# Optimization experiments

Hardware: AMD Instinct MI355X
Metric: run time of the kernel (lower is better)

## Reference

```python
import jax, jax.numpy as jnp
import numpy as np

B, L, D = 2, 2048, 512
DI, N, K, R = 1024, 16, 4, 32  # d_inner=2*d_model, d_state, d_conv, dt_rank=ceil(512/16)
CK = 31   # conformer depthwise kernel
DFF = 2048  # feedforward_factor * d_hidden

def _ln(h, g, b):
    m = h.mean(-1, keepdims=True)
    v = ((h - m) ** 2).mean(-1, keepdims=True)
    return (h - m) * jax.lax.rsqrt(v + 1e-5) * g + b

def _dwconv(h, w, b, pad):
    # h: [B,L,C], w: [C,1,K] depthwise kernel
    y = jax.lax.conv_general_dilated(h.transpose(0, 2, 1), w, (1,), [pad],
                                     feature_group_count=h.shape[-1],
                                     dimension_numbers=('NCH', 'OIH', 'NCH'))
    return y.transpose(0, 2, 1) + b

def setup_inputs():
    key = jax.random.key(0)
    ks = jax.random.split(key, 16)
    nrm = lambda k, s, sc=0.02: jax.random.normal(k, s, jnp.float32) * sc
    return {
        'x': jax.random.normal(ks[0], (B, L, D), jnp.float32),
        'ln_g': jnp.ones(D), 'ln_b': jnp.zeros(D),
        'W_in': nrm(ks[1], (D, 2 * DI)),
        'conv_w': nrm(ks[2], (DI, 1, K), 0.1), 'conv_b': jnp.zeros(DI),
        'W_x': nrm(ks[3], (DI, R + 2 * N)),
        'W_dt': nrm(ks[4], (R, DI), 0.1), 'b_dt': nrm(ks[5], (DI,), 0.1),
        'A_log': jnp.log(jnp.broadcast_to(jnp.arange(1, N + 1, dtype=jnp.float32), (DI, N))),
        'Dp': jnp.ones(DI),
        'W_out': nrm(ks[6], (DI, D)),
        'cm_ln_g': jnp.ones(D), 'cm_ln_b': jnp.zeros(D),
        'cm_pw1_w': nrm(ks[7], (D, 2 * D)), 'cm_pw1_b': jnp.zeros(2 * D),
        'cm_dw_w': nrm(ks[8], (D, 1, CK), 0.1), 'cm_dw_b': jnp.zeros(D),
        'cm_pw2_w': nrm(ks[9], (D, D)), 'cm_pw2_b': jnp.zeros(D),
        'ff_W1': nrm(ks[10], (D, DFF)), 'ff_b1': jnp.zeros(DFF),
        'ff_W2': nrm(ks[11], (DFF, D)), 'ff_b2': jnp.zeros(D),
    }

def _forward(x, ln_g, ln_b, W_in, conv_w, conv_b, W_x, W_dt, b_dt, A_log, Dp, W_out,
             cm_ln_g, cm_ln_b, cm_pw1_w, cm_pw1_b, cm_dw_w, cm_dw_b, cm_pw2_w, cm_pw2_b,
             ff_W1, ff_b1, ff_W2, ff_b2):
    # --- pre LayerNorm ---
    h = _ln(x, ln_g, ln_b)
    # --- Mamba block ---
    xz = h @ W_in                       # [B,L,2*DI]
    xi, z = xz[..., :DI], xz[..., DI:]
    xc = jax.nn.silu(_dwconv(xi, conv_w, conv_b, (K - 1, 0)))  # causal depthwise conv
    dbl = xc @ W_x                      # [B,L,R+2N]
    dt, Bm, Cm = dbl[..., :R], dbl[..., R:R + N], dbl[..., R + N:]
    delta = jax.nn.softplus(dt @ W_dt + b_dt)           # [B,L,DI]
    A = -jnp.exp(A_log)                                  # [DI,N]
    dA = jnp.exp(delta[..., None] * A)                   # [B,L,DI,N]
    dBu = (delta * xc)[..., None] * Bm[:, :, None, :]    # [B,L,DI,N]
    def step(hs, inp):
        a, bu, c = inp
        hs = a * hs + bu                                 # [B,DI,N]
        return hs, jnp.einsum('bdn,bn->bd', hs, c)
    h0 = jnp.zeros((x.shape[0], DI, N), x.dtype)
    _, ys = jax.lax.scan(step, h0, (dA.transpose(1, 0, 2, 3), dBu.transpose(1, 0, 2, 3), Cm.transpose(1, 0, 2)))
    y = ys.transpose(1, 0, 2) + Dp * xc
    y = y * jax.nn.silu(z)
    m = y @ W_out                                        # [B,L,D]
    # --- Conformer-style conv module (residual) ---
    c = _ln(m, cm_ln_g, cm_ln_b)
    c = c @ cm_pw1_w + cm_pw1_b
    a_, g_ = jnp.split(c, 2, axis=-1)
    c = a_ * jax.nn.sigmoid(g_)  # GLU
    c = jax.nn.silu(_dwconv(c, cm_dw_w, cm_dw_b, ((CK - 1) // 2, (CK - 1) // 2)))
    c = c @ cm_pw2_w + cm_pw2_b
    m = m + c
    # --- post LayerNorm (shared params) + FFN (residual) ---
    f = _ln(m, ln_g, ln_b)
    out = f + (jax.nn.gelu(f @ ff_W1 + ff_b1) @ ff_W2 + ff_b2)
    return out

def reference(x, ln_g, ln_b, W_in, conv_w, conv_b, W_x, W_dt, b_dt, A_log, Dp, W_out,
              cm_ln_g, cm_ln_b, cm_pw1_w, cm_pw1_b, cm_dw_w, cm_dw_b, cm_pw2_w, cm_pw2_b,
              ff_W1, ff_b1, ff_W2, ff_b2):
    return _forward(x, ln_g, ln_b, W_in, conv_w, conv_b, W_x, W_dt, b_dt, A_log, Dp, W_out,
                    cm_ln_g, cm_ln_b, cm_pw1_w, cm_pw1_b, cm_dw_w, cm_dw_b, cm_pw2_w, cm_pw2_b,
                    ff_W1, ff_b1, ff_W2, ff_b2)
```

## Files before the change

### kernel.cpp

```cpp
#include <hip/hip_runtime.h>
#include <hip/hip_bf16.h>
#include <math.h>

#define Bc   2
#define Lc   2048
#define Dc   512
#define DIc  1024
#define Nc   16
#define Kc   4
#define Rc   32
#define CKc  31
#define DFFc 2048
#define Mrows (Bc*Lc)
#define CHUNK  32
#define NCHUNK 64

typedef __hip_bfloat16 bf16;
typedef short bf16x8 __attribute__((ext_vector_type(8)));
typedef float f32x4  __attribute__((ext_vector_type(4)));

__device__ __forceinline__ float sigmoidf_(float x){ return 1.f/(1.f+expf(-x)); }
__device__ __forceinline__ float siluf_(float x){ return x*sigmoidf_(x); }
__device__ __forceinline__ float softplusf_(float x){ return fmaxf(x,0.f)+log1pf(expf(-fabsf(x))); }
__device__ __forceinline__ float geluf_(float x){
    float x3 = x*x*x;
    return 0.5f*x*(1.f+tanhf(0.7978845608028654f*(x+0.044715f*x3)));
}

__device__ __forceinline__ void gload16(const void* g, void* l) {
    __builtin_amdgcn_global_load_lds((const __attribute__((address_space(1))) void*)g,
                                     (__attribute__((address_space(3))) void*)l, 16, 0, 0);
}

template<bool WF, bool WB>
__global__ void ln_kernel(const float* __restrict__ in, const float* __restrict__ g,
                          const float* __restrict__ bb, float* __restrict__ outf,
                          bf16* __restrict__ outb, int D) {
    int row = blockIdx.x;
    const float* x = in + (size_t)row * D;
    float s = 0.f, s2 = 0.f;
    for (int i = threadIdx.x; i < D; i += blockDim.x) { float v = x[i]; s += v; s2 += v*v; }
    #pragma unroll
    for (int off = 32; off; off >>= 1) { s += __shfl_down(s, off); s2 += __shfl_down(s2, off); }
    __shared__ float sh[2][4];
    int wave = threadIdx.x >> 6, lane = threadIdx.x & 63;
    if (lane == 0) { sh[0][wave] = s; sh[1][wave] = s2; }
    __syncthreads();
    if (threadIdx.x == 0) {
        float ts = 0.f, ts2 = 0.f;
        int nw = blockDim.x >> 6;
        for (int w = 0; w < nw; ++w) { ts += sh[0][w]; ts2 += sh[1][w]; }
        sh[0][0] = ts; sh[1][0] = ts2;
    }
    __syncthreads();
    float mean = sh[0][0] / D;
    float var  = sh[1][0] / D - mean*mean;
    float rstd = rsqrtf(var + 1e-5f);
    for (int i = threadIdx.x; i < D; i += blockDim.x) {
        float v = (x[i]-mean)*rstd*g[i] + bb[i];
        if (WF) outf[(size_t)row*D + i] = v;
        if (WB) outb[(size_t)row*D + i] = __float2bfloat16(v);
    }
}

struct PrepPack {
    const float* W[8]; bf16* Wt[8]; int K[8]; int N[8]; int start[9];
    const float* x; const float* lg; const float* lb; bf16* hb;
    int lnStart;
};

__global__ __launch_bounds__(256) void prep_all(PrepPack p) {
    __shared__ float t[32][33];
    __shared__ float sh[2][4];
    int tb = blockIdx.x, tid = threadIdx.x;
    if (tb < p.lnStart) {
        int wi = 0;
        #pragma unroll
        for (int i = 0; i < 7; ++i) if (tb >= p.start[i+1]) wi = i+1;
        int lt = tb - p.start[wi];
        int K = p.K[wi], N = p.N[wi];
        int ntx = N >> 5;
        int bx = lt % ntx, by = lt / ntx;
        const float* W = p.W[wi];
        bf16* Wt = p.Wt[wi];
        int tx = tid & 31, ty = tid >> 5;
        #pragma unroll
        for (int i = 0; i < 32; i += 8)
            t[ty+i][tx] = W[(size_t)(by*32+ty+i)*N + bx*32+tx];
        __syncthreads();
        #pragma unroll
        for (int i = 0; i < 32; i += 8)
            Wt[(size_t)(bx*32+ty+i)*K + by*32+tx] = __float2bfloat16(t[tx][ty+i]);
    } else {
        int row = tb - p.lnStart;
        const float* xr = p.x + (size_t)row * Dc;
        float s = 0.f, s2 = 0.f;
        for (int i = tid; i < Dc; i += 256) { float v = xr[i]; s += v; s2 += v*v; }
        #pragma unroll
        for (int off = 32; off; off >>= 1) { s += __shfl_down(s, off); s2 += __shfl_down(s2, off); }
        int wave = tid >> 6, lane = tid & 63;
        if (lane == 0) { sh[0][wave] = s; sh[1][wave] = s2; }
        __syncthreads();
        if (tid == 0) {
            float ts = 0.f, ts2 = 0.f;
            for (int w = 0; w < 4; ++w) { ts += sh[0][w]; ts2 += sh[1][w]; }
            sh[0][0] = ts; sh[1][0] = ts2;
        }
        __syncthreads();
        float mean = sh[0][0] / Dc;
        float var  = sh[1][0] / Dc - mean*mean;
        float rstd = rsqrtf(var + 1e-5f);
        for (int i = tid; i < Dc; i += 256)
            p.hb[(size_t)row*Dc + i] = __float2bfloat16((xr[i]-mean)*rstd*p.lg[i] + p.lb[i]);
    }
}

template<int BM, int BN, int SPLITK, int ZSEL, int ACT, bool BIAS, bool RES, bool WF32, bool WBF16>
__global__ __launch_bounds__(256) void mgemm(const bf16* __restrict__ A, int lda,
                                             const bf16* __restrict__ Wt,
                                             const float* __restrict__ bias,
                                             const float* __restrict__ res,
                                             float* __restrict__ outf,
                                             bf16* __restrict__ outb,
                                             int M, int N, int K) {
    constexpr int BK = 32;
    constexpr int WM = BM/2, WN = BN/2;
    constexpr int AM = WM/16, AN = WN/16;
    constexpr int AISS = BM/64, BISS = BN/64;
    __shared__ __align__(16) bf16 As[2][BM*BK];
    __shared__ __align__(16) bf16 Bs[2][BN*BK];
    const int tid  = threadIdx.x;
    const int wave = tid >> 6, lane = tid & 63;
    const int r16  = lane & 15, kb = lane >> 4;
    const int gx = gridDim.x;
    const int nwg = gx*gridDim.y;
    const int id  = blockIdx.y*gx + blockIdx.x;
    const int sid = (id & 7)*(nwg >> 3) + (id >> 3);
    const int bm = (sid / gx)*BM, bn = (sid % gx)*BN;
    const int wm = (wave>>1)*WM, wn = (wave&1)*WN;
    const bf16* Wp = Wt;
    float* outfp = outf;
    bf16*  outbp = outb;
    if (ZSEL) {
        Wp += (size_t)blockIdx.z*N*K;
        if (WF32)  outfp += (size_t)blockIdx.z*M*N;
        if (WBF16) outbp += (size_t)blockIdx.z*M*N;
    }
    const int Keff = K / SPLITK;
    const int kz0  = (SPLITK > 1) ? blockIdx.z * Keff : 0;
    f32x4 acc[AM][AN] = {};
    const int nt = Keff / BK;

    auto stage = [&](int buf, int kt) {
        #pragma unroll
        for (int it = 0; it < AISS; ++it) {
            int base = (wave*AISS + it) << 10;
            int Lb   = base + (lane << 4);
            int row  = Lb >> 6;
            int gch  = ((Lb >> 4) & 3) ^ (row & 3);
            gload16(A + (size_t)(bm + row)*lda + kz0 + kt*BK + gch*8, (char*)As[buf] + base);
        }
        #pragma unroll
        for (int it = 0; it < BISS; ++it) {
            int base = (wave*BISS + it) << 10;
            int Lb   = base + (lane << 4);
            int row  = Lb >> 6;
            int gch  = ((Lb >> 4) & 3) ^ (row & 3);
            gload16(Wp + (size_t)(bn + row)*K + kz0 + kt*BK + gch*8, (char*)Bs[buf] + base);
        }
    };

    stage(0, 0);
    __syncthreads();
    for (int t = 0; t < nt; ++t) {
        int cur = t & 1;
        if (t + 1 < nt) stage(cur ^ 1, t + 1);
        bf16x8 af[AM], bfr[AN];
        #pragma unroll
        for (int mi = 0; mi < AM; ++mi) {
            int r = wm + mi*16 + r16;
            af[mi] = *(const bf16x8*)((const char*)As[cur] + r*64 + ((kb ^ (r & 3)) << 4));
        }
        #pragma unroll
        for (int ni = 0; ni < AN; ++ni) {
            int r = wn + ni*16 + r16;
            bfr[ni] = *(const bf16x8*)((const char*)Bs[cur] + r*64 + ((kb ^ (r & 3)) << 4));
        }
        #pragma unroll
        for (int mi = 0; mi < AM; ++mi)
            #pragma unroll
            for (int ni = 0; ni < AN; ++ni)
                acc[mi][ni] = __builtin_amdgcn_mfma_f32_16x16x32_bf16(af[mi], bfr[ni], acc[mi][ni], 0, 0, 0);
        __syncthreads();
    }

    #pragma unroll
    for (int mi = 0; mi < AM; ++mi) {
        #pragma unroll
        for (int ni = 0; ni < AN; ++ni) {
            #pragma unroll
            for (int r = 0; r < 4; ++r) {
                int grow = bm + wm + mi*16 + kb*4 + r;
                int gcol = bn + wn + ni*16 + r16;
                float v = acc[mi][ni][r];
                if (SPLITK > 1) {
                    outf[(size_t)blockIdx.z*M*N + (size_t)grow*N + gcol] = v;
                } else {
                    if (BIAS) v += bias[gcol];
                    if (ACT == 1) v = softplusf_(v);
                    else if (ACT == 2) v = geluf_(v);
                    if (RES) v += res[(size_t)grow*N + gcol];
                    if (WF32)  outfp[(size_t)grow*N + gcol] = v;
                    if (WBF16) outbp[(size_t)grow*N + gcol] = __float2bfloat16(v);
                }
            }
        }
    }
}

template<int ACT, bool BIAS, bool RES, bool WF32, bool WBF16>
__global__ __launch_bounds__(256) void wgemm(const bf16* __restrict__ A, int lda,
                                             const bf16* __restrict__ Wt,
                                             const float* __restrict__ bias,
                                             const float* __restrict__ res,
                                             float* __restrict__ outf,
                                             bf16* __restrict__ outb,
                                             int M, int N, int K) {
    constexpr int BM = 64, BN = 64, BK = 32;
    __shared__ __align__(16) char lds[65536];
    const int tid  = threadIdx.x;
    const int wave = tid >> 6, lane = tid & 63;
    const int r16  = lane & 15, kb = lane >> 4;
    const int gx = gridDim.x;
    const int nwg = gx*gridDim.y;
    const int id  = blockIdx.y*gx + blockIdx.x;
    const int sid = (id & 7)*(nwg >> 3) + (id >> 3);
    const int bm = (sid / gx)*BM, bn = (sid % gx)*BN;
    const int Kw  = K >> 2;
    const int k0w = wave * Kw;
    const int nt  = Kw / BK;
    char* myL = lds + wave*16384;
    f32x4 acc[4][4] = {};

    auto stage = [&](int buf, int kt) {
        #pragma unroll
        for (int it = 0; it < 4; ++it) {
            int base = it << 10;
            int Lb   = base + (lane << 4);
            int row  = Lb >> 6;
            int gch  = ((Lb >> 4) & 3) ^ (row & 3);
            gload16(A + (size_t)(bm + row)*lda + k0w + kt*BK + gch*8, myL + buf*8192 + base);
        }
        #pragma unroll
        for (int it = 0; it < 4; ++it) {
            int base = it << 10;
            int Lb   = base + (lane << 4);
            int row  = Lb >> 6;
            int gch  = ((Lb >> 4) & 3) ^ (row & 3);
            gload16(Wt + (size_t)(bn + row)*K + k0w + kt*BK + gch*8, myL + buf*8192 + 4096 + base);
        }
    };

    stage(0, 0);
    for (int t = 0; t < nt; ++t) {
        int cur = t & 1;
        if (t + 1 < nt) {
            stage(cur ^ 1, t + 1);
            asm volatile("s_waitcnt vmcnt(8)" ::: "memory");
        } else {
            asm volatile("s_waitcnt vmcnt(0)" ::: "memory");
        }
        __builtin_amdgcn_sched_barrier(0);
        const char* bufA = myL + cur*8192;
        const char* bufB = bufA + 4096;
        bf16x8 af[4], bfr[4];
        #pragma unroll
        for (int mi = 0; mi < 4; ++mi) {
            int r = mi*16 + r16;
            af[mi] = *(const bf16x8*)(bufA + r*64 + ((kb ^ (r & 3)) << 4));
        }
        #pragma unroll
        for (int ni = 0; ni < 4; ++ni) {
            int r = ni*16 + r16;
            bfr[ni] = *(const bf16x8*)(bufB + r*64 + ((kb ^ (r & 3)) << 4));
        }
        #pragma unroll
        for (int mi = 0; mi < 4; ++mi)
            #pragma unroll
            for (int ni = 0; ni < 4; ++ni)
                acc[mi][ni] = __builtin_amdgcn_mfma_f32_16x16x32_bf16(af[mi], bfr[ni], acc[mi][ni], 0, 0, 0);
    }

    __syncthreads();
    float* red = (float*)lds;
    #pragma unroll
    for (int mi = 0; mi < 4; ++mi) {
        #pragma unroll
        for (int ni = 0; ni < 4; ++ni) {
            int row0 = mi*16 + kb*4;
            int col  = ni*16 + r16;
            #pragma unroll
            for (int r = 0; r < 4; ++r)
                red[wave*4096 + (row0+r)*64 + col] = acc[mi][ni][r];
        }
    }
    __syncthreads();
    #pragma unroll
    for (int i = 0; i < 16; ++i) {
        int o = i*256 + tid;
        int row = o >> 6, col = o & 63;
        float v = red[o] + red[4096+o] + red[8192+o] + red[12288+o];
        int grow = bm + row, gcol = bn + col;
        if (BIAS) v += bias[gcol];
        if (ACT == 1) v = softplusf_(v);
        else if (ACT == 2) v = geluf_(v);
        if (RES) v += res[(size_t)grow*N + gcol];
        if (WF32)  outf[(size_t)grow*N + gcol] = v;
        if (WBF16) outb[(size_t)grow*N + gcol] = __float2bfloat16(v);
    }
}

__global__ void splitk_combine(const float* __restrict__ part, float* __restrict__ outf,
                               bf16* __restrict__ outb, int n, int parts) {
    int i = blockIdx.x*256 + threadIdx.x;
    if (i >= n) return;
    float s = 0.f;
    for (int p = 0; p < parts; ++p) s += part[(size_t)p*n + i];
    outf[i] = s;
    outb[i] = __float2bfloat16(s);
}

template<int T>
__global__ __launch_bounds__(256) void causal_conv_silu(const bf16* __restrict__ xi, const float* __restrict__ w,
                                                        const float* __restrict__ bias,
                                                        bf16* __restrict__ xcb) {
    int d  = blockIdx.x*256 + threadIdx.x;
    int b  = blockIdx.y;
    int l0 = blockIdx.z*T;
    const bf16* src = xi + (size_t)b*Lc*DIc + d;
    float wt[Kc];
    #pragma unroll
    for (int k = 0; k < Kc; ++k) wt[k] = w[d*Kc + k];
    float win[T + Kc - 1];
    #pragma unroll
    for (int i = 0; i < T + Kc - 1; ++i) {
        int li = l0 - (Kc-1) + i;
        win[i] = (li >= 0) ? __bfloat162float(src[(size_t)li*DIc]) : 0.f;
    }
    float bv = bias[d];
    size_t obase = (size_t)b*Lc*DIc + (size_t)l0*DIc + d;
    #pragma unroll
    for (int o = 0; o < T; ++o) {
        float acc = bv;
        #pragma unroll
        for (int k = 0; k < Kc; ++k) acc = fmaf(win[o+k], wt[k], acc);
        xcb[obase + (size_t)o*DIc] = __float2bfloat16(siluf_(acc));
    }
}

__global__ __launch_bounds__(256) void scan_pass1(const float* __restrict__ delta, const bf16* __restrict__ xc,
                                                  const float* __restrict__ dbl, const float* __restrict__ A_log,
                                                  float* __restrict__ P, float* __restrict__ H) {
    int dgroup = blockIdx.x & 3;
    int bci = blockIdx.x >> 2;
    int b = bci & 1, chunk = bci >> 1;
    int d = dgroup*256 + threadIdx.x;
    float Av[16];
    #pragma unroll
    for (int j = 0; j < 4; ++j) {
        f32x4 v = *(const f32x4*)(&A_log[d*16 + 4*j]);
        #pragma unroll
        for (int q = 0; q < 4; ++q) Av[4*j+q] = -__expf(v[q]);
    }
    float h[16], Pl[16];
    #pragma unroll
    for (int n = 0; n < 16; ++n) { h[n] = 0.f; Pl[n] = 1.f; }
    size_t row0 = (size_t)b*Lc + (size_t)chunk*CHUNK;
    for (int i = 0; i < CHUNK; ++i) {
        size_t rowi = row0 + i;
        float dv  = delta[rowi*DIc + d];
        float xcv = __bfloat162float(xc[rowi*DIc + d]);
        float dxc = dv*xcv;
        f32x4 B0 = *(const f32x4*)(&dbl[rowi*64 + Rc + 0]);
        f32x4 B1 = *(const f32x4*)(&dbl[rowi*64 + Rc + 4]);
        f32x4 B2 = *(const f32x4*)(&dbl[rowi*64 + Rc + 8]);
        f32x4 B3 = *(const f32x4*)(&dbl[rowi*64 + Rc + 12]);
        float Bv[16];
        #pragma unroll
        for (int q = 0; q < 4; ++q) { Bv[q]=B0[q]; Bv[4+q]=B1[q]; Bv[8+q]=B2[q]; Bv[12+q]=B3[q]; }
        #pragma unroll
        for (int n = 0; n < 16; ++n) {
            float a = __expf(dv*Av[n]);
            h[n] = fmaf(a, h[n], dxc*Bv[n]);
            Pl[n] *= a;
        }
    }
    size_t pidx = ((size_t)chunk*2048 + (size_t)b*DIc + d) * 16;
    #pragma unroll
    for (int j = 0; j < 4; ++j) {
        f32x4 vp, vh;
        #pragma unroll
        for (int q = 0; q < 4; ++q) { vp[q] = Pl[4*j+q]; vh[q] = h[4*j+q]; }
        *(f32x4*)(&P[pidx + 4*j]) = vp;
        *(f32x4*)(&H[pidx + 4*j]) = vh;
    }
}

__global__ void scan_combine(float* __restrict__ P, const float* __restrict__ H) {
    int t = blockIdx.x*blockDim.x + threadIdx.x;
    float h = 0.f;
    #pragma unroll
    for (int c = 0; c < NCHUNK; ++c) {
        size_t idx = (size_t)c*32768 + t;
        float Pv = P[idx], Hv = H[idx];
        P[idx] = h;
        h = fmaf(Pv, h, Hv);
    }
}

__global__ __launch_bounds__(256) void scan_pass3(const float* __restrict__ delta, const bf16* __restrict__ xc,
                                                  const float* __restrict__ dbl, const bf16* __restrict__ z,
                                                  const float* __restrict__ A_log, const float* __restrict__ Dp,
                                                  const float* __restrict__ hstart, bf16* __restrict__ y) {
    int dgroup = blockIdx.x & 3;
    int bci = blockIdx.x >> 2;
    int b = bci & 1, chunk = bci >> 1;
    int d = dgroup*256 + threadIdx.x;
    float Av[16];
    #pragma unroll
    for (int j = 0; j < 4; ++j) {
        f32x4 v = *(const f32x4*)(&A_log[d*16 + 4*j]);
        #pragma unroll
        for (int q = 0; q < 4; ++q) Av[4*j+q] = -__expf(v[q]);
    }
    float Dv = Dp[d];
    float h[16];
    size_t pidx = ((size_t)chunk*2048 + (size_t)b*DIc + d) * 16;
    #pragma unroll
    for (int j = 0; j < 4; ++j) {
        f32x4 v = *(const f32x4*)(&hstart[pidx + 4*j]);
        #pragma unroll
        for (int q = 0; q < 4; ++q) h[4*j+q] = v[q];
    }
    size_t row0 = (size_t)b*Lc + (size_t)chunk*CHUNK;
    for (int i = 0; i < CHUNK; ++i) {
        size_t rowi = row0 + i;
        float dv  = delta[rowi*DIc + d];
        float xcv = __bfloat162float(xc[rowi*DIc + d]);
        float dxc = dv*xcv;
        f32x4 B0 = *(const f32x4*)(&dbl[rowi*64 + Rc + 0]);
        f32x4 B1 = *(const f32x4*)(&dbl[rowi*64 + Rc + 4]);
        f32x4 B2 = *(const f32x4*)(&dbl[rowi*64 + Rc + 8]);
        f32x4 B3 = *(const f32x4*)(&dbl[rowi*64 + Rc + 12]);
        f32x4 C0 = *(const f32x4*)(&dbl[rowi*64 + Rc + Nc + 0]);
        f32x4 C1 = *(const f32x4*)(&dbl[rowi*64 + Rc + Nc + 4]);
        f32x4 C2 = *(const f32x4*)(&dbl[rowi*64 + Rc + Nc + 8]);
        f32x4 C3 = *(const f32x4*)(&dbl[rowi*64 + Rc + Nc + 12]);
        float Bv[16], Cv[16];
        #pragma unroll
        for (int q = 0; q < 4; ++q) {
            Bv[q]=B0[q]; Bv[4+q]=B1[q]; Bv[8+q]=B2[q]; Bv[12+q]=B3[q];
            Cv[q]=C0[q]; Cv[4+q]=C1[q]; Cv[8+q]=C2[q]; Cv[12+q]=C3[q];
        }
        float s0=0.f, s1=0.f, s2=0.f, s3=0.f;
        #pragma unroll
        for (int n = 0; n < 16; ++n) {
            float a = __expf(dv*Av[n]);
            h[n] = fmaf(a, h[n], dxc*Bv[n]);
        }
        #pragma unroll
        for (int j = 0; j < 4; ++j) {
            s0 = fmaf(h[4*j+0], Cv[4*j+0], s0);
            s1 = fmaf(h[4*j+1], Cv[4*j+1], s1);
            s2 = fmaf(h[4*j+2], Cv[4*j+2], s2);
            s3 = fmaf(h[4*j+3], Cv[4*j+3], s3);
        }
        float contrib = (s0+s1)+(s2+s3);
        float zv = __bfloat162float(z[rowi*DIc + d]);
        y[rowi*DIc + d] = __float2bfloat16((contrib + Dv*xcv) * siluf_(zv));
    }
}

template<int T>
__global__ __launch_bounds__(256) void sym_conv_glu_silu(const bf16* __restrict__ c2, const float* __restrict__ w,
                                                         const float* __restrict__ bias, bf16* __restrict__ out) {
    int d  = blockIdx.x*256 + threadIdx.x;
    int b  = blockIdx.y;
    int l0 = blockIdx.z*T;
    const bf16* base = c2 + (size_t)b*Lc*(2*Dc) + d;
    float wt[CKc];
    #pragma unroll
    for (int k = 0; k < CKc; ++k) wt[k] = w[d*CKc + k];
    constexpr int HALF = (CKc-1)/2;
    float win[T + CKc - 1];
    #pragma unroll
    for (int i = 0; i < T + CKc - 1; ++i) {
        int li = l0 - HALF + i;
        if (li >= 0 && li < Lc) {
            float a = __bfloat162float(base[(size_t)li*(2*Dc)]);
            float g = __bfloat162float(base[(size_t)li*(2*Dc) + Dc]);
            win[i] = a * sigmoidf_(g);
        } else win[i] = 0.f;
    }
    float bv = bias[d];
    size_t obase = (size_t)b*Lc*Dc + (size_t)l0*Dc + d;
    #pragma unroll
    for (int o = 0; o < T; ++o) {
        float acc = bv;
        #pragma unroll
        for (int k = 0; k < CKc; ++k) acc = fmaf(win[o+k], wt[k], acc);
        out[obase + (size_t)o*Dc] = __float2bfloat16(siluf_(acc));
    }
}

extern "C" void kernel_launch(void* const* d_in, const int* in_sizes, int n_in,
                              void* d_out, int out_size, void* d_ws, size_t ws_size,
                              hipStream_t stream) {
    const float* x      = (const float*)d_in[0];
    const float* ln_g   = (const float*)d_in[1];
    const float* ln_b   = (const float*)d_in[2];
    const float* W_in   = (const float*)d_in[3];
    const float* conv_w = (const float*)d_in[4];
    const float* conv_b = (const float*)d_in[5];
    const float* W_x    = (const float*)d_in[6];
    const float* W_dt   = (const float*)d_in[7];
    const float* b_dt   = (const float*)d_in[8];
    const float* A_log  = (const float*)d_in[9];
    const float* Dp     = (const float*)d_in[10];
    const float* W_out  = (const float*)d_in[11];
    const float* cm_ln_g= (const float*)d_in[12];
    const float* cm_ln_b= (const float*)d_in[13];
    const float* pw1_w  = (const float*)d_in[14];
    const float* pw1_b  = (const float*)d_in[15];
    const float* dw_w   = (const float*)d_in[16];
    const float* dw_b   = (const float*)d_in[17];
    const float* pw2_w  = (const float*)d_in[18];
    const float* pw2_b  = (const float*)d_in[19];
    const float* ff_W1  = (const float*)d_in[20];
    const float* ff_b1  = (const float*)d_in[21];
    const float* ff_W2  = (const float*)d_in[22];
    const float* ff_b2  = (const float*)d_in[23];
    float* out = (float*)d_out;
    float* ws  = (float*)d_ws;

    float* A_  = ws;
    float* A2_ = ws + 4194304;
    float* B_  = ws + 8388608;
    float* C_  = ws + 12582912;
    float* D_  = ws + 12845056;
    float* F_  = ws + 17039360;
    float* H_  = ws + 18612224;
    float* J_  = ws + 20709376;

    bf16*  xib     = (bf16*)A_;
    bf16*  zb      = xib + (size_t)Mrows*DIc;
    float* part_buf= A_;
    bf16*  c2b     = (bf16*)A_;
    float* P_buf   = A2_;
    float* H_buf   = A2_ + 2097152;
    bf16*  g1b     = (bf16*)B_;
    float* dbl_buf = C_;
    float* dl_buf  = D_;
    float* m_buf   = D_;
    bf16*  dblb    = (bf16*)F_;
    bf16*  cb      = (bf16*)F_;
    bf16*  ccb     = (bf16*)F_;
    bf16*  fb      = (bf16*)F_;
    bf16*  hb      = (bf16*)H_;
    bf16*  xcb     = (bf16*)H_;
    bf16*  yb      = (bf16*)H_;
    float* f_buf   = out;

    bf16* Jw = (bf16*)J_;
    bf16* Win_t  = Jw;
    bf16* Wx_t   = Jw + 1048576;
    bf16* Wdt_t  = Jw + 1114112;
    bf16* Wout_t = Jw + 1146880;
    bf16* pw1_t  = Jw + 1671168;
    bf16* pw2_t  = Jw + 2195456;
    bf16* ffW1_t = Jw + 2457600;
    bf16* ffW2_t = Jw + 3506176;

    const int M = Mrows;

    {
        PrepPack p;
        const float* Ws[8] = {W_in, W_x, W_dt, W_out, pw1_w, pw2_w, ff_W1, ff_W2};
        bf16* Ts[8] = {Win_t, Wx_t, Wdt_t, Wout_t, pw1_t, pw2_t, ffW1_t, ffW2_t};
        int Ks[8] = {512, 1024, 32, 1024, 512, 512, 512, 2048};
        int Ns[8] = {2048, 64, 1024, 512, 1024, 512, 2048, 512};
        int acc = 0;
        for (int i = 0; i < 8; ++i) {
            p.W[i] = Ws[i]; p.Wt[i] = Ts[i]; p.K[i] = Ks[i]; p.N[i] = Ns[i];
            p.start[i] = acc;
            acc += (Ns[i]/32)*(Ks[i]/32);
        }
        p.start[8] = acc;
        p.lnStart = acc;
        p.x = x; p.lg = ln_g; p.lb = ln_b; p.hb = hb;
        prep_all<<<acc + M, 256, 0, stream>>>(p);
    }

    mgemm<128,64,1,1,0,false,false,false,true><<<dim3(1024/64, M/128, 2), 256, 0, stream>>>(
        hb, Dc, Win_t, nullptr, nullptr, nullptr, xib, M, DIc, Dc);
    causal_conv_silu<16><<<dim3(DIc/256, Bc, Lc/16), 256, 0, stream>>>(xib, conv_w, conv_b, xcb);
    mgemm<64,64,8,0,0,false,false,true,false><<<dim3(64/64, M/64, 8), 256, 0, stream>>>(
        xcb, DIc, Wx_t, nullptr, nullptr, part_buf, nullptr, M, 64, DIc);
    splitk_combine<<<(M*64+255)/256, 256, 0, stream>>>(part_buf, dbl_buf, dblb, M*64, 8);
    mgemm<64,64,1,0,1,true,false,true,false><<<dim3(1024/64, M/64), 256, 0, stream>>>(
        dblb, 64, Wdt_t, b_dt, nullptr, dl_buf, nullptr, M, DIc, Rc);
    scan_pass1<<<512, 256, 0, stream>>>(dl_buf, xcb, dbl_buf, A_log, P_buf, H_buf);
    scan_combine<<<128, 256, 0, stream>>>(P_buf, H_buf);
    scan_pass3<<<512, 256, 0, stream>>>(dl_buf, xcb, dbl_buf, zb, A_log, Dp, P_buf, yb);
    wgemm<0,false,false,true,false><<<dim3(512/64, M/64), 256, 0, stream>>>(
        yb, DIc, Wout_t, nullptr, nullptr, m_buf, nullptr, M, Dc, DIc);
    ln_kernel<false,true><<<M, 256, 0, stream>>>(m_buf, cm_ln_g, cm_ln_b, nullptr, cb, Dc);
    mgemm<128,64,1,0,0,true,false,false,true><<<dim3(1024/64, M/128), 256, 0, stream>>>(
        cb, Dc, pw1_t, pw1_b, nullptr, nullptr, c2b, M, 2*Dc, Dc);
    sym_conv_glu_silu<16><<<dim3(Dc/256, Bc, Lc/16), 256, 0, stream>>>(c2b, dw_w, dw_b, ccb);
    wgemm<0,true,true,true,false><<<dim3(512/64, M/64), 256, 0, stream>>>(
        ccb, Dc, pw2_t, pw2_b, m_buf, m_buf, nullptr, M, Dc, Dc);
    ln_kernel<true,true><<<M, 256, 0, stream>>>(m_buf, ln_g, ln_b, f_buf, fb, Dc);
    mgemm<128,64,1,0,2,true,false,false,true><<<dim3(2048/64, M/128), 256, 0, stream>>>(
        fb, Dc, ffW1_t, ff_b1, nullptr, nullptr, g1b, M, DFFc, Dc);
    wgemm<0,true,true,true,false><<<dim3(512/64, M/64), 256, 0, stream>>>(
        g1b, DFFc, ffW2_t, ff_b2, f_buf, out, nullptr, M, Dc, DFFc);
}
```

Measured before the change: 240.0 us.

## Fuse three scan kernels into one cooperative kernel with grid syncs

Replaces the separate scan_pass1, scan_combine and scan_pass3 launches with a single cooperative kernel that uses grid-wide syncs between phases. The output y is written in place over the xc buffer. The aim is to remove two kernel launch gaps and tail effects. The cost is two grid barriers, the cooperative launch requirement that all 512 blocks be co-resident, and only 128 blocks doing work in the middle phase. A ZSEL template parameter is added to wgemm but is unused (always 0).

```diff
diff --git a/kernel.cpp b/kernel.cpp
--- a/kernel.cpp
+++ b/kernel.cpp
@@ -1,6 +1,9 @@
 #include <hip/hip_runtime.h>
 #include <hip/hip_bf16.h>
+#include <hip/hip_cooperative_groups.h>
 #include <math.h>
+
+namespace cg = cooperative_groups;
 
 #define Bc   2
 #define Lc   2048
@@ -218,7 +221,7 @@
     }
 }
 
-template<int ACT, bool BIAS, bool RES, bool WF32, bool WBF16>
+template<int ZSEL, int ACT, bool BIAS, bool RES, bool WF32, bool WBF16>
 __global__ __launch_bounds__(256) void wgemm(const bf16* __restrict__ A, int lda,
                                              const bf16* __restrict__ Wt,
                                              const float* __restrict__ bias,
@@ -236,6 +239,15 @@
     const int id  = blockIdx.y*gx + blockIdx.x;
     const int sid = (id & 7)*(nwg >> 3) + (id >> 3);
     const int bm = (sid / gx)*BM, bn = (sid % gx)*BN;
+    const bf16* Wp = Wt;
+    float* outfp = outf;
+    bf16*  outbp = outb;
+    const float* resp = res;
+    if (ZSEL) {
+        Wp += (size_t)blockIdx.z*N*K;
+        if (WF32)  outfp += (size_t)blockIdx.z*M*N;
+        if (WBF16) outbp += (size_t)blockIdx.z*M*N;
+    }
     const int Kw  = K >> 2;
     const int k0w = wave * Kw;
     const int nt  = Kw / BK;
@@ -257,7 +269,7 @@
             int Lb   = base + (lane << 4);
             int row  = Lb >> 6;
             int gch  = ((Lb >> 4) & 3) ^ (row & 3);
-            gload16(Wt + (size_t)(bn + row)*K + k0w + kt*BK + gch*8, myL + buf*8192 + 4096 + base);
+            gload16(Wp + (size_t)(bn + row)*K + k0w + kt*BK + gch*8, myL + buf*8192 + 4096 + base);
         }
     };
 
@@ -314,9 +326,9 @@
         if (BIAS) v += bias[gcol];
         if (ACT == 1) v = softplusf_(v);
         else if (ACT == 2) v = geluf_(v);
-        if (RES) v += res[(size_t)grow*N + gcol];
-        if (WF32)  outf[(size_t)grow*N + gcol] = v;
-        if (WBF16) outb[(size_t)grow*N + gcol] = __float2bfloat16(v);
+        if (RES) v += resp[(size_t)grow*N + gcol];
+        if (WF32)  outfp[(size_t)grow*N + gcol] = v;
+        if (WBF16) outbp[(size_t)grow*N + gcol] = __float2bfloat16(v);
     }
 }
 
@@ -358,8 +370,9 @@
     }
 }
 
-__global__ __launch_bounds__(256) void scan_pass1(const float* __restrict__ delta, const bf16* __restrict__ xc,
-                                                  const float* __restrict__ dbl, const float* __restrict__ A_log,
+__global__ __launch_bounds__(256) void scan_fused(const float* __restrict__ delta, bf16* __restrict__ xcy,
+                                                  const float* __restrict__ dbl, const bf16* __restrict__ z,
+                                                  const float* __restrict__ A_log, const float* __restrict__ Dp,
                                                   float* __restrict__ P, float* __restrict__ H) {
     int dgroup = blockIdx.x & 3;
     int bci = blockIdx.x >> 2;
@@ -372,112 +385,101 @@
         #pragma unroll
         for (int q = 0; q < 4; ++q) Av[4*j+q] = -__expf(v[q]);
     }
-    float h[16], Pl[16];
-    #pragma unroll
-    for (int n = 0; n < 16; ++n) { h[n] = 0.f; Pl[n] = 1.f; }
     size_t row0 = (size_t)b*Lc + (size_t)chunk*CHUNK;
-    for (int i = 0; i < CHUNK; ++i) {
-        size_t rowi = row0 + i;
-        float dv  = delta[rowi*DIc + d];
-        float xcv = __bfloat162float(xc[rowi*DIc + d]);
-        float dxc = dv*xcv;
-        f32x4 B0 = *(const f32x4*)(&dbl[rowi*64 + Rc + 0]);
-        f32x4 B1 = *(const f32x4*)(&dbl[rowi*64 + Rc + 4]);
-        f32x4 B2 = *(const f32x4*)(&dbl[rowi*64 + Rc + 8]);
-        f32x4 B3 = *(const f32x4*)(&dbl[rowi*64 + Rc + 12]);
-        float Bv[16];
-        #pragma unroll
-        for (int q = 0; q < 4; ++q) { Bv[q]=B0[q]; Bv[4+q]=B1[q]; Bv[8+q]=B2[q]; Bv[12+q]=B3[q]; }
-        #pragma unroll
-        for (int n = 0; n < 16; ++n) {
-            float a = __expf(dv*Av[n]);
-            h[n] = fmaf(a, h[n], dxc*Bv[n]);
-            Pl[n] *= a;
-        }
-    }
     size_t pidx = ((size_t)chunk*2048 + (size_t)b*DIc + d) * 16;
-    #pragma unroll
-    for (int j = 0; j < 4; ++j) {
-        f32x4 vp, vh;
-        #pragma unroll
-        for (int q = 0; q < 4; ++q) { vp[q] = Pl[4*j+q]; vh[q] = h[4*j+q]; }
-        *(f32x4*)(&P[pidx + 4*j]) = vp;
-        *(f32x4*)(&H[pidx + 4*j]) = vh;
-    }
-}
-
-__global__ void scan_combine(float* __restrict__ P, const float* __restrict__ H) {
-    int t = blockIdx.x*blockDim.x + threadIdx.x;
-    float h = 0.f;
-    #pragma unroll
-    for (int c = 0; c < NCHUNK; ++c) {
-        size_t idx = (size_t)c*32768 + t;
-        float Pv = P[idx], Hv = H[idx];
-        P[idx] = h;
-        h = fmaf(Pv, h, Hv);
-    }
-}
-
-__global__ __launch_bounds__(256) void scan_pass3(const float* __restrict__ delta, const bf16* __restrict__ xc,
-                                                  const float* __restrict__ dbl, const bf16* __restrict__ z,
-                                                  const float* __restrict__ A_log, const float* __restrict__ Dp,
-                                                  const float* __restrict__ hstart, bf16* __restrict__ y) {
-    int dgroup = blockIdx.x & 3;
-    int bci = blockIdx.x >> 2;
-    int b = bci & 1, chunk = bci >> 1;
-    int d = dgroup*256 + threadIdx.x;
-    float Av[16];
-    #pragma unroll
-    for (int j = 0; j < 4; ++j) {
-        f32x4 v = *(const f32x4*)(&A_log[d*16 + 4*j]);
-        #pragma unroll
-        for (int q = 0; q < 4; ++q) Av[4*j+q] = -__expf(v[q]);
-    }
-    float Dv = Dp[d];
-    float h[16];
-    size_t pidx = ((size_t)chunk*2048 + (size_t)b*DIc + d) * 16;
-    #pragma unroll
-    for (int j = 0; j < 4; ++j) {
-        f32x4 v = *(const f32x4*)(&hstart[pidx + 4*j]);
-        #pragma unroll
-        for (int q = 0; q < 4; ++q) h[4*j+q] = v[q];
-    }
-    size_t row0 = (size_t)b*Lc + (size_t)chunk*CHUNK;
-    for (int i = 0; i < CHUNK; ++i) {
-        size_t rowi = row0 + i;
-        float dv  = delta[rowi*DIc + d];
-        float xcv = __bfloat162float(xc[rowi*DIc + d]);
-        float dxc = dv*xcv;
-        f32x4 B0 = *(const f32x4*)(&dbl[rowi*64 + Rc + 0]);
-        f32x4 B1 = *(const f32x4*)(&dbl[rowi*64 + Rc + 4]);
-        f32x4 B2 = *(const f32x4*)(&dbl[rowi*64 + Rc + 8]);
-        f32x4 B3 = *(const f32x4*)(&dbl[rowi*64 + Rc + 12]);
-        f32x4 C0 = *(const f32x4*)(&dbl[rowi*64 + Rc + Nc + 0]);
-        f32x4 C1 = *(const f32x4*)(&dbl[rowi*64 + Rc + Nc + 4]);
-        f32x4 C2 = *(const f32x4*)(&dbl[rowi*64 + Rc + Nc + 8]);
-        f32x4 C3 = *(const f32x4*)(&dbl[rowi*64 + Rc + Nc + 12]);
-        float Bv[16], Cv[16];
-        #pragma unroll
-        for (int q = 0; q < 4; ++q) {
-            Bv[q]=B0[q]; Bv[4+q]=B1[q]; Bv[8+q]=B2[q]; Bv[12+q]=B3[q];
-            Cv[q]=C0[q]; Cv[4+q]=C1[q]; Cv[8+q]=C2[q]; Cv[12+q]=C3[q];
-        }
-        float s0=0.f, s1=0.f, s2=0.f, s3=0.f;
-        #pragma unroll
-        for (int n = 0; n < 16; ++n) {
-            float a = __expf(dv*Av[n]);
-            h[n] = fmaf(a, h[n], dxc*Bv[n]);
+
+    {
+        float h[16], Pl[16];
+        #pragma unroll
+        for (int n = 0; n < 16; ++n) { h[n] = 0.f; Pl[n] = 1.f; }
+        for (int i = 0; i < CHUNK; ++i) {
+            size_t rowi = row0 + i;
+            float dv  = delta[rowi*DIc + d];
+            float xcv = __bfloat162float(xcy[rowi*DIc + d]);
+            float dxc = dv*xcv;
+            f32x4 B0 = *(const f32x4*)(&dbl[rowi*64 + Rc + 0]);
+            f32x4 B1 = *(const f32x4*)(&dbl[rowi*64 + Rc + 4]);
+            f32x4 B2 = *(const f32x4*)(&dbl[rowi*64 + Rc + 8]);
+            f32x4 B3 = *(const f32x4*)(&dbl[rowi*64 + Rc + 12]);
+            float Bv[16];
+            #pragma unroll
+            for (int q = 0; q < 4; ++q) { Bv[q]=B0[q]; Bv[4+q]=B1[q]; Bv[8+q]=B2[q]; Bv[12+q]=B3[q]; }
+            #pragma unroll
+            for (int n = 0; n < 16; ++n) {
+                float a = __expf(dv*Av[n]);
+                h[n] = fmaf(a, h[n], dxc*Bv[n]);
+                Pl[n] *= a;
+            }
         }
         #pragma unroll
         for (int j = 0; j < 4; ++j) {
-            s0 = fmaf(h[4*j+0], Cv[4*j+0], s0);
-            s1 = fmaf(h[4*j+1], Cv[4*j+1], s1);
-            s2 = fmaf(h[4*j+2], Cv[4*j+2], s2);
-            s3 = fmaf(h[4*j+3], Cv[4*j+3], s3);
-        }
-        float contrib = (s0+s1)+(s2+s3);
-        float zv = __bfloat162float(z[rowi*DIc + d]);
-        y[rowi*DIc + d] = __float2bfloat16((contrib + Dv*xcv) * siluf_(zv));
+            f32x4 vp, vh;
+            #pragma unroll
+            for (int q = 0; q < 4; ++q) { vp[q] = Pl[4*j+q]; vh[q] = h[4*j+q]; }
+            *(f32x4*)(&P[pidx + 4*j]) = vp;
+            *(f32x4*)(&H[pidx + 4*j]) = vh;
+        }
+    }
+    cg::this_grid().sync();
+
+    if (blockIdx.x < 128) {
+        int t = blockIdx.x*256 + threadIdx.x;
+        float hh = 0.f;
+        #pragma unroll
+        for (int c = 0; c < NCHUNK; ++c) {
+            size_t idx = (size_t)c*32768 + t;
+            float Pv = P[idx], Hv = H[idx];
+            P[idx] = hh;
+            hh = fmaf(Pv, hh, Hv);
+        }
+    }
+    cg::this_grid().sync();
+
+    {
+        float Dv = Dp[d];
+        float h[16];
+        #pragma unroll
+        for (int j = 0; j < 4; ++j) {
+            f32x4 v = *(const f32x4*)(&P[pidx + 4*j]);
+            #pragma unroll
+            for (int q = 0; q < 4; ++q) h[4*j+q] = v[q];
+        }
+        for (int i = 0; i < CHUNK; ++i) {
+            size_t rowi = row0 + i;
+            float dv  = delta[rowi*DIc + d];
+            float xcv = __bfloat162float(xcy[rowi*DIc + d]);
+            float dxc = dv*xcv;
+            f32x4 B0 = *(const f32x4*)(&dbl[rowi*64 + Rc + 0]);
+            f32x4 B1 = *(const f32x4*)(&dbl[rowi*64 + Rc + 4]);
+            f32x4 B2 = *(const f32x4*)(&dbl[rowi*64 + Rc + 8]);
+            f32x4 B3 = *(const f32x4*)(&dbl[rowi*64 + Rc + 12]);
+            f32x4 C0 = *(const f32x4*)(&dbl[rowi*64 + Rc + Nc + 0]);
+            f32x4 C1 = *(const f32x4*)(&dbl[rowi*64 + Rc + Nc + 4]);
+            f32x4 C2 = *(const f32x4*)(&dbl[rowi*64 + Rc + Nc + 8]);
+            f32x4 C3 = *(const f32x4*)(&dbl[rowi*64 + Rc + Nc + 12]);
+            float Bv[16], Cv[16];
+            #pragma unroll
+            for (int q = 0; q < 4; ++q) {
+                Bv[q]=B0[q]; Bv[4+q]=B1[q]; Bv[8+q]=B2[q]; Bv[12+q]=B3[q];
+                Cv[q]=C0[q]; Cv[4+q]=C1[q]; Cv[8+q]=C2[q]; Cv[12+q]=C3[q];
+            }
+            float s0=0.f, s1=0.f, s2=0.f, s3=0.f;
+            #pragma unroll
+            for (int n = 0; n < 16; ++n) {
+                float a = __expf(dv*Av[n]);
+                h[n] = fmaf(a, h[n], dxc*Bv[n]);
+            }
+            #pragma unroll
+            for (int j = 0; j < 4; ++j) {
+                s0 = fmaf(h[4*j+0], Cv[4*j+0], s0);
+                s1 = fmaf(h[4*j+1], Cv[4*j+1], s1);
+                s2 = fmaf(h[4*j+2], Cv[4*j+2], s2);
+                s3 = fmaf(h[4*j+3], Cv[4*j+3], s3);
+            }
+            float contrib = (s0+s1)+(s2+s3);
+            float zv = __bfloat162float(z[rowi*DIc + d]);
+            xcy[rowi*DIc + d] = __float2bfloat16((contrib + Dv*xcv) * siluf_(zv));
+        }
     }
 }
 
@@ -568,7 +570,6 @@
     bf16*  fb      = (bf16*)F_;
     bf16*  hb      = (bf16*)H_;
     bf16*  xcb     = (bf16*)H_;
-    bf16*  yb      = (bf16*)H_;
     float* f_buf   = out;
 
     bf16* Jw = (bf16*)J_;
@@ -609,20 +610,25 @@
     splitk_combine<<<(M*64+255)/256, 256, 0, stream>>>(part_buf, dbl_buf, dblb, M*64, 8);
     mgemm<64,64,1,0,1,true,false,true,false><<<dim3(1024/64, M/64), 256, 0, stream>>>(
         dblb, 64, Wdt_t, b_dt, nullptr, dl_buf, nullptr, M, DIc, Rc);
-    scan_pass1<<<512, 256, 0, stream>>>(dl_buf, xcb, dbl_buf, A_log, P_buf, H_buf);
-    scan_combine<<<128, 256, 0, stream>>>(P_buf, H_buf);
-    scan_pass3<<<512, 256, 0, stream>>>(dl_buf, xcb, dbl_buf, zb, A_log, Dp, P_buf, yb);
-    wgemm<0,false,false,true,false><<<dim3(512/64, M/64), 256, 0, stream>>>(
-        yb, DIc, Wout_t, nullptr, nullptr, m_buf, nullptr, M, Dc, DIc);
+    {
+        const float* dl_c = dl_buf; bf16* xcy = xcb; const float* dbl_c = dbl_buf;
+        const bf16* z_c = zb; const float* al_c = A_log; const float* dp_c = Dp;
+        float* P_c = P_buf; float* H_c = H_buf;
+        void* args[] = { (void*)&dl_c, (void*)&xcy, (void*)&dbl_c, (void*)&z_c,
+                         (void*)&al_c, (void*)&dp_c, (void*)&P_c, (void*)&H_c };
+        hipLaunchCooperativeKernel((void*)scan_fused, dim3(512), dim3(256), args, 0, stream);
+    }
+    wgemm<0,0,false,false,true,false><<<dim3(512/64, M/64), 256, 0, stream>>>(
+        xcb, DIc, Wout_t, nullptr, nullptr, m_buf, nullptr, M, Dc, DIc);
     ln_kernel<false,true><<<M, 256, 0, stream>>>(m_buf, cm_ln_g, cm_ln_b, nullptr, cb, Dc);
     mgemm<128,64,1,0,0,true,false,false,true><<<dim3(1024/64, M/128), 256, 0, stream>>>(
         cb, Dc, pw1_t, pw1_b, nullptr, nullptr, c2b, M, 2*Dc, Dc);
     sym_conv_glu_silu<16><<<dim3(Dc/256, Bc, Lc/16), 256, 0, stream>>>(c2b, dw_w, dw_b, ccb);
-    wgemm<0,true,true,true,false><<<dim3(512/64, M/64), 256, 0, stream>>>(
+    wgemm<0,0,true,true,true,false><<<dim3(512/64, M/64), 256, 0, stream>>>(
         ccb, Dc, pw2_t, pw2_b, m_buf, m_buf, nullptr, M, Dc, Dc);
     ln_kernel<true,true><<<M, 256, 0, stream>>>(m_buf, ln_g, ln_b, f_buf, fb, Dc);
     mgemm<128,64,1,0,2,true,false,false,true><<<dim3(2048/64, M/128), 256, 0, stream>>>(
         fb, Dc, ffW1_t, ff_b1, nullptr, nullptr, g1b, M, DFFc, Dc);
-    wgemm<0,true,true,true,false><<<dim3(512/64, M/64), 256, 0, stream>>>(
+    wgemm<0,0,true,true,true,false><<<dim3(512/64, M/64), 256, 0, stream>>>(
         g1b, DFFc, ffW2_t, ff_b2, f_buf, out, nullptr, M, Dc, DFFc);
 }
```

Result: slower. 402.2 us (+67.6%).
